# Kernel optimization log

Measured on AMD Instinct MI355X. Metric: run time of the kernel, lower is better.

The kernel has to match this reference:

```python
import math
import jax, jax.numpy as jnp
import numpy as np

B, T, H = 4096, 49, 512

def setup_inputs() -> dict:
    key = jax.random.key(0)
    ks = jax.random.split(key, 13)
    sc = 1.0 / math.sqrt(H)
    return {
        "v": jax.random.normal(ks[0], (B, T, H), dtype=jnp.float32),
        "h": jax.random.normal(ks[1], (B, H), dtype=jnp.float32),
        "s": jax.random.normal(ks[2], (B, H), dtype=jnp.float32),
        "W_h": jax.random.normal(ks[3], (H, H), dtype=jnp.float32) * sc,
        "b_h": jax.random.normal(ks[4], (H,), dtype=jnp.float32) * sc,
        "W_v": jax.random.normal(ks[5], (H, H), dtype=jnp.float32) * sc,
        "b_v": jax.random.normal(ks[6], (H,), dtype=jnp.float32) * sc,
        "w_z": jax.random.normal(ks[7], (H,), dtype=jnp.float32) * sc,
        "b_z": jax.random.normal(ks[8], (), dtype=jnp.float32) * sc,
        "W_s": jax.random.normal(ks[9], (H, H), dtype=jnp.float32) * sc,
        "b_s": jax.random.normal(ks[10], (H,), dtype=jnp.float32) * sc,
        "w_beta": jax.random.normal(ks[11], (H,), dtype=jnp.float32) * sc,
        "b_beta": jax.random.normal(ks[12], (), dtype=jnp.float32) * sc,
    }

def reference(v, h, s, W_h, b_h, W_v, b_v, w_z, b_z, W_s, b_s, w_beta, b_beta):
    # eval mode: dropout is identity
    h_proj = h @ W_h + b_h                                  # [B, H]
    v_proj = jnp.einsum('bth,hk->btk', v, W_v) + b_v        # [B, T, H]
    z = jnp.tanh(h_proj[:, None, :] + v_proj)               # [B, T, H]
    z = jnp.einsum('bth,h->bt', z, w_z) + b_z               # [B, T]
    beta = jnp.tanh((s @ W_s + b_s + h_proj) * math.sqrt(0.5))  # [B, H]
    beta = (beta @ w_beta + b_beta)[:, None]                # [B, 1]
    a = jax.nn.softmax(jnp.concatenate([z, beta], axis=1), axis=1)  # [B, T+1]
    v_ext = jnp.concatenate([v, s[:, None, :]], axis=1)     # [B, T+1, H]
    c = jnp.einsum('bt,bth->bh', a, v_ext)                  # [B, H]
    return c
```

## Files before the change

kernel.cpp:

```cpp
#include <hip/hip_runtime.h>
#include <stdint.h>

#define B_ 4096
#define T_ 49
#define H_ 512
#define BT_ (B_*T_)

typedef __bf16 bf16x8 __attribute__((ext_vector_type(8)));
typedef float  f32x4  __attribute__((ext_vector_type(4)));
typedef unsigned short ushort_;

__device__ __forceinline__ ushort_ f2bf(float f){
  unsigned int u = __float_as_uint(f);
  u += 0x7fffu + ((u >> 16) & 1u);
  return (ushort_)(u >> 16);
}
__device__ __forceinline__ float bf2f(ushort_ u){
  return __uint_as_float(((unsigned int)u) << 16);
}
__device__ __forceinline__ float fast_tanh(float x){
  float e = __expf(2.0f * x);
  return 1.0f - 2.0f * __builtin_amdgcn_rcpf(e + 1.0f);
}

__global__ __launch_bounds__(256) void k_pack3(
    const float* __restrict__ Wv, const float* __restrict__ Wh,
    const float* __restrict__ Ws, ushort_* __restrict__ bpack,
    ushort_* __restrict__ whp, ushort_* __restrict__ wsp){
  const int grp = blockIdx.x >> 7;
  const float* W = (grp==0) ? Wv : (grp==1) ? Wh : Ws;
  ushort_* pack  = (grp==0) ? bpack : (grp==1) ? whp : wsp;
  int idx = (blockIdx.x & 127) * 256 + threadIdx.x;
  int lane = idx & 63;
  int gt   = (idx >> 6) & 31;
  int kk   = idx >> 11;
  int col  = gt*16 + (lane & 15);
  int k0   = kk*32 + (lane >> 4)*8;
  ushort4 lo, hi;
  lo.x = f2bf(W[(k0+0)*H_ + col]);
  lo.y = f2bf(W[(k0+1)*H_ + col]);
  lo.z = f2bf(W[(k0+2)*H_ + col]);
  lo.w = f2bf(W[(k0+3)*H_ + col]);
  hi.x = f2bf(W[(k0+4)*H_ + col]);
  hi.y = f2bf(W[(k0+5)*H_ + col]);
  hi.z = f2bf(W[(k0+6)*H_ + col]);
  hi.w = f2bf(W[(k0+7)*H_ + col]);
  ushort4* dst = (ushort4*)pack;
  dst[idx*2]   = lo;
  dst[idx*2+1] = hi;
}

__global__ __launch_bounds__(256) void k_proj2(
    const float* __restrict__ h, const float* __restrict__ s,
    const ushort_* __restrict__ whp, const ushort_* __restrict__ wsp,
    const float* __restrict__ bh, const float* __restrict__ bs,
    const float* __restrict__ bv, const float* __restrict__ wbeta,
    const float* __restrict__ bbeta_p,
    float* __restrict__ hpb, float* __restrict__ beta)
{
  __shared__ __align__(16) ushort_ hl[16*H_];
  __shared__ __align__(16) ushort_ sl[16*H_];
  __shared__ float zwp[4][16];
  const int tid = threadIdx.x;
  const int w = tid >> 6, lane = tid & 63;
  const int l15 = lane & 15, l4 = lane >> 4;
  const int b0 = blockIdx.x * 16;

  {
    const int r = tid >> 4;
    const float4* hsrc = (const float4*)(h + (size_t)(b0+r)*H_);
    const float4* ssrc = (const float4*)(s + (size_t)(b0+r)*H_);
    #pragma unroll
    for(int p=0;p<8;p++){
      int q  = (tid & 15) + p*16;
      int k0 = q*4;
      float4 fh = hsrc[q];
      float4 fs = ssrc[q];
      int idx = (k0>>5)*512 + ((((k0&31)>>3)<<4) + r)*8 + (k0&7);
      ushort4 uh; uh.x=f2bf(fh.x); uh.y=f2bf(fh.y); uh.z=f2bf(fh.z); uh.w=f2bf(fh.w);
      ushort4 us; us.x=f2bf(fs.x); us.y=f2bf(fs.y); us.z=f2bf(fs.z); us.w=f2bf(fs.w);
      *(ushort4*)&hl[idx] = uh;
      *(ushort4*)&sl[idx] = us;
    }
  }
  __syncthreads();

  const bf16x8* __restrict__ bph = (const bf16x8*)whp;
  const bf16x8* __restrict__ bps = (const bf16x8*)wsp;
  const int bbase = w*512 + lane;

  f32x4 acch[8], accs[8];
  #pragma unroll
  for(int ni=0;ni<8;ni++){ acch[ni]=(f32x4){0,0,0,0}; accs[ni]=(f32x4){0,0,0,0}; }

  #pragma unroll 2
  for(int kk=0;kk<16;kk++){
    bf16x8 ah = *(const bf16x8*)&hl[kk*512 + lane*8];
    bf16x8 as2 = *(const bf16x8*)&sl[kk*512 + lane*8];
    #pragma unroll
    for(int ni=0;ni<8;ni++){
      acch[ni] = __builtin_amdgcn_mfma_f32_16x16x32_bf16(ah,  bph[kk*2048 + bbase + ni*64], acch[ni], 0,0,0);
      accs[ni] = __builtin_amdgcn_mfma_f32_16x16x32_bf16(as2, bps[kk*2048 + bbase + ni*64], accs[ni], 0,0,0);
    }
  }

  float bhv[8], bsv[8], bvv[8], wbv[8];
  #pragma unroll
  for(int ni=0;ni<8;ni++){
    int col = w*128 + ni*16 + l15;
    bhv[ni] = bh[col]; bsv[ni] = bs[col]; bvv[ni] = bv[col]; wbv[ni] = wbeta[col];
  }
  float btsum[4];
  #pragma unroll
  for(int rr=0;rr<4;rr++){
    int row = l4*4 + rr;
    float bsum = 0.f;
    #pragma unroll
    for(int ni=0;ni<8;ni++){
      int col = w*128 + ni*16 + l15;
      float hp = acch[ni][rr] + bhv[ni];
      hpb[(size_t)(b0+row)*H_ + col] = hp + bvv[ni];
      float bt = fast_tanh((accs[ni][rr] + bsv[ni] + hp) * 0.70710678118654752f);
      bsum = fmaf(bt, wbv[ni], bsum);
    }
    btsum[rr] = bsum;
  }
  #pragma unroll
  for(int rr=0;rr<4;rr++){
    btsum[rr] += __shfl_xor(btsum[rr], 1);
    btsum[rr] += __shfl_xor(btsum[rr], 2);
    btsum[rr] += __shfl_xor(btsum[rr], 4);
    btsum[rr] += __shfl_xor(btsum[rr], 8);
    if(l15 == 0) zwp[w][l4*4+rr] = btsum[rr];
  }
  __syncthreads();
  if(tid < 16)
    beta[b0+tid] = zwp[0][tid] + zwp[1][tid] + zwp[2][tid] + zwp[3][tid] + bbeta_p[0];
}

__global__ __launch_bounds__(256, 2) void k_fused(
    const float* __restrict__ v, const ushort_* __restrict__ bpack,
    const float* __restrict__ hpb, const float* __restrict__ wz,
    const float* __restrict__ bz_p, const float* __restrict__ beta,
    const float* __restrict__ s, float* __restrict__ out)
{
  __shared__ __align__(16) ushort_ Av[T_*H_];
  __shared__ float zw[4][64];
  __shared__ float a_s[64];
  const int tid = threadIdx.x;
  const int w = tid >> 6, lane = tid & 63;
  const int l15 = lane & 15, l4 = lane >> 4;
  const int b = blockIdx.x;

  const f32x4* __restrict__ vsrc = (const f32x4*)(v + (size_t)b * T_ * H_);
  const bf16x8* __restrict__ bp = (const bf16x8*)bpack;
  const int bbase = w*256 + lane;

  const int srow = tid >> 4, c4 = tid & 15;
  const int slot = ((c4 >> 1) ^ (srow & 7));
  const int wsub = ((c4 & 1) << 3);
  const bool r48 = (tid < 16);

#define VLOAD(N0,N1,N2,N3, CH) { \
    N0 = __builtin_nontemporal_load(vsrc + (srow     )*128 + (CH)*16 + c4); \
    N1 = __builtin_nontemporal_load(vsrc + (srow + 16)*128 + (CH)*16 + c4); \
    N2 = __builtin_nontemporal_load(vsrc + (srow + 32)*128 + (CH)*16 + c4); \
    if(r48) N3 = __builtin_nontemporal_load(vsrc + 48*128 + (CH)*16 + c4); }

#define SWRITE(N0,N1,N2,N3, CH) { \
    const int cb_ = (CH)*128; ushort4 u_; \
    u_.x=f2bf(N0[0]); u_.y=f2bf(N0[1]); u_.z=f2bf(N0[2]); u_.w=f2bf(N0[3]); \
    *(ushort4*)((char*)Av + (srow   )*1024 + cb_ + (slot<<4) + wsub) = u_; \
    u_.x=f2bf(N1[0]); u_.y=f2bf(N1[1]); u_.z=f2bf(N1[2]); u_.w=f2bf(N1[3]); \
    *(ushort4*)((char*)Av + (srow+16)*1024 + cb_ + (slot<<4) + wsub) = u_; \
    u_.x=f2bf(N2[0]); u_.y=f2bf(N2[1]); u_.z=f2bf(N2[2]); u_.w=f2bf(N2[3]); \
    *(ushort4*)((char*)Av + (srow+32)*1024 + cb_ + (slot<<4) + wsub) = u_; \
    if(r48){ \
      u_.x=f2bf(N3[0]); u_.y=f2bf(N3[1]); u_.z=f2bf(N3[2]); u_.w=f2bf(N3[3]); \
      *(ushort4*)((char*)Av + 48*1024 + cb_ + (slot<<4) + wsub) = u_; } }

#define AFRAG(af, KS) { \
    _Pragma("unroll") \
    for(int mi=0;mi<4;mi++){ \
      int row_ = (mi < 3) ? (mi*16 + l15) : 48; \
      int g_   = ((KS)*4 + l4) ^ (row_ & 7); \
      af[mi] = *(const bf16x8*)((const char*)Av + row_*1024 + (g_<<4)); } }

#define MFMA16(af, bfr) { \
    __builtin_amdgcn_s_setprio(1); \
    _Pragma("unroll") \
    for(int mi=0;mi<4;mi++) \
      _Pragma("unroll") \
      for(int ni=0;ni<4;ni++) \
        acc[mi][ni] = __builtin_amdgcn_mfma_f32_16x16x32_bf16(af[mi], bfr[ni], acc[mi][ni], 0,0,0); \
    __builtin_amdgcn_s_setprio(0); }

  {
    f32x4 A0,A1,A2,A3, B0,B1,B2,B3;
    VLOAD(A0,A1,A2,A3, 0)
    #pragma unroll
    for(int cc=0; cc<4; cc++){
      VLOAD(B0,B1,B2,B3, 2*cc+1)
      SWRITE(A0,A1,A2,A3, 2*cc)
      if(cc < 3) VLOAD(A0,A1,A2,A3, 2*cc+2)
      SWRITE(B0,B1,B2,B3, 2*cc+1)
    }
  }

  f32x4 acc[4][4];
  bf16x8 bq[4][4];
  bf16x8 af2[2][4];

  #pragma unroll
  for(int mi=0;mi<4;mi++)
    #pragma unroll
    for(int ni=0;ni<4;ni++) acc[mi][ni] = (f32x4){0.f,0.f,0.f,0.f};

  #pragma unroll
  for(int p=0;p<4;p++)
    #pragma unroll
    for(int ni=0;ni<4;ni++) bq[p][ni] = bp[p*2048 + bbase + ni*64];

  __syncthreads();

  AFRAG(af2[0], 0)
  #pragma unroll
  for(int kk=0; kk<16; kk++){
    if(kk < 15){ AFRAG(af2[(kk+1)&1], kk+1) }
    MFMA16(af2[kk&1], bq[kk&3])
    if(kk < 12){
      #pragma unroll
      for(int ni=0;ni<4;ni++) bq[kk&3][ni] = bp[(kk+4)*2048 + bbase + ni*64];
    }
  }

  {
    float wzv[4], hp0[4];
    #pragma unroll
    for(int ni=0;ni<4;ni++){
      int col = w*64 + ni*16 + l15;
      wzv[ni] = wz[col];
      hp0[ni] = hpb[(size_t)b*H_ + col];
    }
    float zp[16];
    #pragma unroll
    for(int mi=0;mi<4;mi++)
      #pragma unroll
      for(int r=0;r<4;r++){
        float az = 0.f;
        #pragma unroll
        for(int ni=0;ni<4;ni++)
          az = fmaf(fast_tanh(acc[mi][ni][r] + hp0[ni]), wzv[ni], az);
        zp[mi*4+r] = az;
      }
    #pragma unroll
    for(int i=0;i<16;i++){
      zp[i] += __shfl_xor(zp[i], 1);
      zp[i] += __shfl_xor(zp[i], 2);
      zp[i] += __shfl_xor(zp[i], 4);
      zp[i] += __shfl_xor(zp[i], 8);
    }
    if(l15 == 0){
      #pragma unroll
      for(int mi=0;mi<4;mi++)
        #pragma unroll
        for(int r=0;r<4;r++)
          zw[w][mi*16 + l4*4 + r] = zp[mi*4+r];
    }
  }

  #pragma unroll
  for(int mi=0;mi<4;mi++)
    #pragma unroll
    for(int ni=0;ni<4;ni++) acc[mi][ni] = (f32x4){0.f,0.f,0.f,0.f};

  #pragma unroll
  for(int p=0;p<4;p++)
    #pragma unroll
    for(int ni=0;ni<4;ni++) bq[p][ni] = bp[p*2048 + 1024 + bbase + ni*64];

  AFRAG(af2[0], 0)
  #pragma unroll
  for(int kk=0; kk<16; kk++){
    if(kk < 15){ AFRAG(af2[(kk+1)&1], kk+1) }
    MFMA16(af2[kk&1], bq[kk&3])
    if(kk < 12){
      #pragma unroll
      for(int ni=0;ni<4;ni++) bq[kk&3][ni] = bp[(kk+4)*2048 + 1024 + bbase + ni*64];
    }
  }

  {
    float wzv[4], hp0[4];
    #pragma unroll
    for(int ni=0;ni<4;ni++){
      int col = 256 + w*64 + ni*16 + l15;
      wzv[ni] = wz[col];
      hp0[ni] = hpb[(size_t)b*H_ + col];
    }
    float zp[16];
    #pragma unroll
    for(int mi=0;mi<4;mi++)
      #pragma unroll
      for(int r=0;r<4;r++){
        float az = 0.f;
        #pragma unroll
        for(int ni=0;ni<4;ni++)
          az = fmaf(fast_tanh(acc[mi][ni][r] + hp0[ni]), wzv[ni], az);
        zp[mi*4+r] = az;
      }
    #pragma unroll
    for(int i=0;i<16;i++){
      zp[i] += __shfl_xor(zp[i], 1);
      zp[i] += __shfl_xor(zp[i], 2);
      zp[i] += __shfl_xor(zp[i], 4);
      zp[i] += __shfl_xor(zp[i], 8);
    }
    if(l15 == 0){
      #pragma unroll
      for(int mi=0;mi<4;mi++)
        #pragma unroll
        for(int r=0;r<4;r++)
          zw[w][mi*16 + l4*4 + r] += zp[mi*4+r];
    }
  }
  __syncthreads();

  if(tid < 64){
    float zv;
    if(tid < T_)       zv = zw[0][tid] + zw[1][tid] + zw[2][tid] + zw[3][tid] + bz_p[0];
    else if(tid == T_) zv = beta[b];
    else               zv = -3.0e38f;
    float m = zv;
    #pragma unroll
    for(int off=32;off>=1;off>>=1) m = fmaxf(m, __shfl_xor(m, off));
    float e = (tid <= T_) ? __expf(zv - m) : 0.f;
    float ssum = e;
    #pragma unroll
    for(int off=32;off>=1;off>>=1) ssum += __shfl_xor(ssum, off);
    a_s[tid] = e * __builtin_amdgcn_rcpf(ssum);
  }
  __syncthreads();

  const int n0 = tid * 2;
  float ax = 0.f, ay = 0.f;
  #pragma unroll 7
  for(int t=0;t<T_;t++){
    float at = a_s[t];
    unsigned int u = *(const unsigned int*)((const char*)Av + t*1024
                       + ((((n0>>3) ^ (t&7)))<<4) + ((n0&7)<<1));
    float x = __uint_as_float((u & 0xFFFFu) << 16);
    float y = __uint_as_float(u & 0xFFFF0000u);
    ax = fmaf(at, x, ax);
    ay = fmaf(at, y, ay);
  }
  float a49 = a_s[T_];
  float2 sv = ((const float2*)(s + (size_t)b*H_))[tid];
  ax = fmaf(a49, sv.x, ax);
  ay = fmaf(a49, sv.y, ay);
  float2 res; res.x = ax; res.y = ay;
  ((float2*)(out + (size_t)b*H_))[tid] = res;
}

extern "C" void kernel_launch(void* const* d_in, const int* in_sizes, int n_in,
                              void* d_out, int out_size, void* d_ws, size_t ws_size,
                              hipStream_t stream)
{
  const float* v   = (const float*)d_in[0];
  const float* h   = (const float*)d_in[1];
  const float* s   = (const float*)d_in[2];
  const float* Wh  = (const float*)d_in[3];
  const float* bh  = (const float*)d_in[4];
  const float* Wv  = (const float*)d_in[5];
  const float* bv  = (const float*)d_in[6];
  const float* wz  = (const float*)d_in[7];
  const float* bz  = (const float*)d_in[8];
  const float* Ws  = (const float*)d_in[9];
  const float* bs  = (const float*)d_in[10];
  const float* wb  = (const float*)d_in[11];
  const float* bbet= (const float*)d_in[12];
  float* out = (float*)d_out;

  float* hpb  = (float*)d_ws;
  float* beta = hpb + (size_t)B_*H_;
  ushort_* bpack = (ushort_*)(beta + B_);
  ushort_* whp   = bpack + (size_t)H_*H_;
  ushort_* wsp   = whp   + (size_t)H_*H_;

  k_pack3<<<384, 256, 0, stream>>>(Wv, Wh, Ws, bpack, whp, wsp);
  k_proj2<<<B_/16, 256, 0, stream>>>(h, s, whp, wsp, bh, bs, bv, wb, bbet, hpb, beta);
  k_fused<<<B_, 256, 0, stream>>>(v, bpack, hpb, wz, bz, beta, s, out);
}
```

Measured before the change: 220.3 us.

## Make fused kernel persistent with double-buffered LDS prefetch of next batch's v

Result: slower. 692.5 us (+214.3%).

```diff
diff --git a/kernel.cpp b/kernel.cpp
--- a/kernel.cpp
+++ b/kernel.cpp
@@ -5,6 +5,7 @@
 #define T_ 49
 #define H_ 512
 #define BT_ (B_*T_)
+#define PB_ (T_*H_)
 
 typedef __bf16 bf16x8 __attribute__((ext_vector_type(8)));
 typedef float  f32x4  __attribute__((ext_vector_type(4)));
@@ -138,228 +139,228 @@
     beta[b0+tid] = zwp[0][tid] + zwp[1][tid] + zwp[2][tid] + zwp[3][tid] + bbeta_p[0];
 }
 
-__global__ __launch_bounds__(256, 2) void k_fused(
+__global__ __launch_bounds__(256, 1) void k_fused(
     const float* __restrict__ v, const ushort_* __restrict__ bpack,
     const float* __restrict__ hpb, const float* __restrict__ wz,
     const float* __restrict__ bz_p, const float* __restrict__ beta,
     const float* __restrict__ s, float* __restrict__ out)
 {
-  __shared__ __align__(16) ushort_ Av[T_*H_];
+  __shared__ __align__(16) ushort_ Av[2*PB_];
   __shared__ float zw[4][64];
   __shared__ float a_s[64];
   const int tid = threadIdx.x;
   const int w = tid >> 6, lane = tid & 63;
   const int l15 = lane & 15, l4 = lane >> 4;
-  const int b = blockIdx.x;
-
-  const f32x4* __restrict__ vsrc = (const f32x4*)(v + (size_t)b * T_ * H_);
+  const int blk = blockIdx.x;
+  const bool t128 = (tid < 128);
+
   const bf16x8* __restrict__ bp = (const bf16x8*)bpack;
   const int bbase = w*256 + lane;
 
-  const int srow = tid >> 4, c4 = tid & 15;
-  const int slot = ((c4 >> 1) ^ (srow & 7));
-  const int wsub = ((c4 & 1) << 3);
-  const bool r48 = (tid < 16);
-
-#define VLOAD(N0,N1,N2,N3, CH) { \
-    N0 = __builtin_nontemporal_load(vsrc + (srow     )*128 + (CH)*16 + c4); \
-    N1 = __builtin_nontemporal_load(vsrc + (srow + 16)*128 + (CH)*16 + c4); \
-    N2 = __builtin_nontemporal_load(vsrc + (srow + 32)*128 + (CH)*16 + c4); \
-    if(r48) N3 = __builtin_nontemporal_load(vsrc + 48*128 + (CH)*16 + c4); }
-
-#define SWRITE(N0,N1,N2,N3, CH) { \
-    const int cb_ = (CH)*128; ushort4 u_; \
-    u_.x=f2bf(N0[0]); u_.y=f2bf(N0[1]); u_.z=f2bf(N0[2]); u_.w=f2bf(N0[3]); \
-    *(ushort4*)((char*)Av + (srow   )*1024 + cb_ + (slot<<4) + wsub) = u_; \
-    u_.x=f2bf(N1[0]); u_.y=f2bf(N1[1]); u_.z=f2bf(N1[2]); u_.w=f2bf(N1[3]); \
-    *(ushort4*)((char*)Av + (srow+16)*1024 + cb_ + (slot<<4) + wsub) = u_; \
-    u_.x=f2bf(N2[0]); u_.y=f2bf(N2[1]); u_.z=f2bf(N2[2]); u_.w=f2bf(N2[3]); \
-    *(ushort4*)((char*)Av + (srow+32)*1024 + cb_ + (slot<<4) + wsub) = u_; \
-    if(r48){ \
-      u_.x=f2bf(N3[0]); u_.y=f2bf(N3[1]); u_.z=f2bf(N3[2]); u_.w=f2bf(N3[3]); \
-      *(ushort4*)((char*)Av + 48*1024 + cb_ + (slot<<4) + wsub) = u_; } }
-
-#define AFRAG(af, KS) { \
+  float wzv0[4], wzv1[4];
+  #pragma unroll
+  for(int ni=0;ni<4;ni++){
+    wzv0[ni] = wz[      w*64 + ni*16 + l15];
+    wzv1[ni] = wz[256 + w*64 + ni*16 + l15];
+  }
+  const float bzv = bz_p[0];
+
+#define SIDX(J, VI, WB) { \
+    int flat_ = ((J) < 24) ? (tid + (J)*256) : (6144 + tid); \
+    int row_ = flat_ >> 7, c4_ = flat_ & 127; \
+    VI = row_*128 + c4_; \
+    WB = row_*1024 + ((((c4_>>1) ^ (row_&7)))<<4) + ((c4_&1)<<3); }
+
+#define SISSUE(SR, VS, J0, JN) { \
+    _Pragma("unroll") \
+    for(int j=(J0); j<(JN); j++){ \
+      if(j != 24 || t128){ int vi_, wb_; SIDX(j, vi_, wb_) \
+        SR[j-(J0)] = __builtin_nontemporal_load((VS) + vi_); } } }
+
+#define SWR(SR, DST, J0, A, Bn) { \
+    _Pragma("unroll") \
+    for(int j=(A); j<(Bn); j++){ \
+      if((j+(J0)) != 24 || t128){ int vi_, wb_; SIDX(j+(J0), vi_, wb_) \
+        ushort4 u_; u_.x=f2bf(SR[j][0]); u_.y=f2bf(SR[j][1]); \
+        u_.z=f2bf(SR[j][2]); u_.w=f2bf(SR[j][3]); \
+        *(ushort4*)((DST) + wb_) = u_; } } }
+
+#define AFRAG(af, KS, SRC) { \
     _Pragma("unroll") \
     for(int mi=0;mi<4;mi++){ \
       int row_ = (mi < 3) ? (mi*16 + l15) : 48; \
       int g_   = ((KS)*4 + l4) ^ (row_ & 7); \
-      af[mi] = *(const bf16x8*)((const char*)Av + row_*1024 + (g_<<4)); } }
+      af[mi] = *(const bf16x8*)((SRC) + row_*1024 + (g_<<4)); } }
 
 #define MFMA16(af, bfr) { \
-    __builtin_amdgcn_s_setprio(1); \
     _Pragma("unroll") \
     for(int mi=0;mi<4;mi++) \
       _Pragma("unroll") \
       for(int ni=0;ni<4;ni++) \
-        acc[mi][ni] = __builtin_amdgcn_mfma_f32_16x16x32_bf16(af[mi], bfr[ni], acc[mi][ni], 0,0,0); \
-    __builtin_amdgcn_s_setprio(0); }
+        acc[mi][ni] = __builtin_amdgcn_mfma_f32_16x16x32_bf16(af[mi], bfr[ni], acc[mi][ni], 0,0,0); }
+
+#define BLOADP(DST, KK, P) { \
+    _Pragma("unroll") \
+    for(int ni=0;ni<4;ni++) DST[ni] = bp[(KK)*2048 + (P)*1024 + bbase + ni*64]; }
 
   {
-    f32x4 A0,A1,A2,A3, B0,B1,B2,B3;
-    VLOAD(A0,A1,A2,A3, 0)
-    #pragma unroll
-    for(int cc=0; cc<4; cc++){
-      VLOAD(B0,B1,B2,B3, 2*cc+1)
-      SWRITE(A0,A1,A2,A3, 2*cc)
-      if(cc < 3) VLOAD(A0,A1,A2,A3, 2*cc+2)
-      SWRITE(B0,B1,B2,B3, 2*cc+1)
-    }
-  }
-
-  f32x4 acc[4][4];
-  bf16x8 bq[4][4];
-  bf16x8 af2[2][4];
-
-  #pragma unroll
-  for(int mi=0;mi<4;mi++)
-    #pragma unroll
-    for(int ni=0;ni<4;ni++) acc[mi][ni] = (f32x4){0.f,0.f,0.f,0.f};
-
-  #pragma unroll
-  for(int p=0;p<4;p++)
-    #pragma unroll
-    for(int ni=0;ni<4;ni++) bq[p][ni] = bp[p*2048 + bbase + ni*64];
-
+    const f32x4* vs = (const f32x4*)(v + (size_t)(blk*16)*T_*H_);
+    f32x4 pA[12], pBv[13];
+    SISSUE(pA, vs, 0, 12)
+    SISSUE(pBv, vs, 12, 25)
+    SWR(pA, (char*)Av, 0, 0, 12)
+    SWR(pBv, (char*)Av, 12, 0, 13)
+  }
   __syncthreads();
 
-  AFRAG(af2[0], 0)
-  #pragma unroll
-  for(int kk=0; kk<16; kk++){
-    if(kk < 15){ AFRAG(af2[(kk+1)&1], kk+1) }
-    MFMA16(af2[kk&1], bq[kk&3])
-    if(kk < 12){
-      #pragma unroll
-      for(int ni=0;ni<4;ni++) bq[kk&3][ni] = bp[(kk+4)*2048 + bbase + ni*64];
-    }
-  }
-
-  {
-    float wzv[4], hp0[4];
-    #pragma unroll
-    for(int ni=0;ni<4;ni++){
-      int col = w*64 + ni*16 + l15;
-      wzv[ni] = wz[col];
-      hp0[ni] = hpb[(size_t)b*H_ + col];
-    }
-    float zp[16];
+  #pragma unroll 1
+  for(int bi=0; bi<16; bi++){
+    const int b = blk*16 + bi;
+    const char* curc = (const char*)Av + (bi&1)*(PB_*2);
+    char* nxtc = (char*)Av + ((bi+1)&1)*(PB_*2);
+    const f32x4* vsn = (const f32x4*)(v + (size_t)(b+1)*T_*H_);
+    const bool more = (bi < 15);
+
+    f32x4 srA[12], srB[13];
+    f32x4 acc[4][4];
+    bf16x8 bq[2][4], af2[2][4];
+
     #pragma unroll
     for(int mi=0;mi<4;mi++)
       #pragma unroll
-      for(int r=0;r<4;r++){
-        float az = 0.f;
-        #pragma unroll
-        for(int ni=0;ni<4;ni++)
-          az = fmaf(fast_tanh(acc[mi][ni][r] + hp0[ni]), wzv[ni], az);
-        zp[mi*4+r] = az;
-      }
-    #pragma unroll
-    for(int i=0;i<16;i++){
-      zp[i] += __shfl_xor(zp[i], 1);
-      zp[i] += __shfl_xor(zp[i], 2);
-      zp[i] += __shfl_xor(zp[i], 4);
-      zp[i] += __shfl_xor(zp[i], 8);
-    }
-    if(l15 == 0){
+      for(int ni=0;ni<4;ni++) acc[mi][ni] = (f32x4){0.f,0.f,0.f,0.f};
+    BLOADP(bq[0], 0, 0)
+    BLOADP(bq[1], 1, 0)
+    AFRAG(af2[0], 0, curc)
+
+    #pragma unroll
+    for(int kk=0; kk<16; kk++){
+      if(kk < 15){ AFRAG(af2[(kk+1)&1], kk+1, curc) }
+      if(kk == 2 && more){ SISSUE(srA, vsn, 0, 12) }
+      if(kk == 12 && more){ SISSUE(srB, vsn, 12, 25) }
+      MFMA16(af2[kk&1], bq[kk&1])
+      if(kk < 14){ BLOADP(bq[kk&1], kk+2, 0) }
+      if(kk == 8  && more){ SWR(srA, nxtc, 0, 0, 6) }
+      if(kk == 10 && more){ SWR(srA, nxtc, 0, 6, 12) }
+    }
+
+    {
+      float hpv[4];
+      #pragma unroll
+      for(int ni=0;ni<4;ni++) hpv[ni] = hpb[(size_t)b*H_ + w*64 + ni*16 + l15];
+      float zp[16];
       #pragma unroll
       for(int mi=0;mi<4;mi++)
         #pragma unroll
-        for(int r=0;r<4;r++)
-          zw[w][mi*16 + l4*4 + r] = zp[mi*4+r];
-    }
-  }
-
-  #pragma unroll
-  for(int mi=0;mi<4;mi++)
-    #pragma unroll
-    for(int ni=0;ni<4;ni++) acc[mi][ni] = (f32x4){0.f,0.f,0.f,0.f};
-
-  #pragma unroll
-  for(int p=0;p<4;p++)
-    #pragma unroll
-    for(int ni=0;ni<4;ni++) bq[p][ni] = bp[p*2048 + 1024 + bbase + ni*64];
-
-  AFRAG(af2[0], 0)
-  #pragma unroll
-  for(int kk=0; kk<16; kk++){
-    if(kk < 15){ AFRAG(af2[(kk+1)&1], kk+1) }
-    MFMA16(af2[kk&1], bq[kk&3])
-    if(kk < 12){
-      #pragma unroll
-      for(int ni=0;ni<4;ni++) bq[kk&3][ni] = bp[(kk+4)*2048 + 1024 + bbase + ni*64];
-    }
-  }
-
-  {
-    float wzv[4], hp0[4];
-    #pragma unroll
-    for(int ni=0;ni<4;ni++){
-      int col = 256 + w*64 + ni*16 + l15;
-      wzv[ni] = wz[col];
-      hp0[ni] = hpb[(size_t)b*H_ + col];
-    }
-    float zp[16];
+        for(int r=0;r<4;r++){
+          float az = 0.f;
+          #pragma unroll
+          for(int ni=0;ni<4;ni++)
+            az = fmaf(fast_tanh(acc[mi][ni][r] + hpv[ni]), wzv0[ni], az);
+          zp[mi*4+r] = az;
+        }
+      #pragma unroll
+      for(int i=0;i<16;i++){
+        zp[i] += __shfl_xor(zp[i], 1);
+        zp[i] += __shfl_xor(zp[i], 2);
+        zp[i] += __shfl_xor(zp[i], 4);
+        zp[i] += __shfl_xor(zp[i], 8);
+      }
+      if(l15 == 0){
+        #pragma unroll
+        for(int mi=0;mi<4;mi++)
+          #pragma unroll
+          for(int r=0;r<4;r++)
+            zw[w][mi*16 + l4*4 + r] = zp[mi*4+r];
+      }
+    }
+
     #pragma unroll
     for(int mi=0;mi<4;mi++)
       #pragma unroll
-      for(int r=0;r<4;r++){
-        float az = 0.f;
-        #pragma unroll
-        for(int ni=0;ni<4;ni++)
-          az = fmaf(fast_tanh(acc[mi][ni][r] + hp0[ni]), wzv[ni], az);
-        zp[mi*4+r] = az;
-      }
-    #pragma unroll
-    for(int i=0;i<16;i++){
-      zp[i] += __shfl_xor(zp[i], 1);
-      zp[i] += __shfl_xor(zp[i], 2);
-      zp[i] += __shfl_xor(zp[i], 4);
-      zp[i] += __shfl_xor(zp[i], 8);
-    }
-    if(l15 == 0){
+      for(int ni=0;ni<4;ni++) acc[mi][ni] = (f32x4){0.f,0.f,0.f,0.f};
+    BLOADP(bq[0], 0, 1)
+    BLOADP(bq[1], 1, 1)
+    AFRAG(af2[0], 0, curc)
+
+    #pragma unroll
+    for(int kk=0; kk<16; kk++){
+      if(kk < 15){ AFRAG(af2[(kk+1)&1], kk+1, curc) }
+      MFMA16(af2[kk&1], bq[kk&1])
+      if(kk < 14){ BLOADP(bq[kk&1], kk+2, 1) }
+      if(kk == 2 && more){ SWR(srB, nxtc, 12, 0, 5) }
+      if(kk == 4 && more){ SWR(srB, nxtc, 12, 5, 9) }
+      if(kk == 6 && more){ SWR(srB, nxtc, 12, 9, 13) }
+    }
+
+    {
+      float hpv[4];
+      #pragma unroll
+      for(int ni=0;ni<4;ni++) hpv[ni] = hpb[(size_t)b*H_ + 256 + w*64 + ni*16 + l15];
+      float zp[16];
       #pragma unroll
       for(int mi=0;mi<4;mi++)
         #pragma unroll
-        for(int r=0;r<4;r++)
-          zw[w][mi*16 + l4*4 + r] += zp[mi*4+r];
-    }
-  }
-  __syncthreads();
-
-  if(tid < 64){
-    float zv;
-    if(tid < T_)       zv = zw[0][tid] + zw[1][tid] + zw[2][tid] + zw[3][tid] + bz_p[0];
-    else if(tid == T_) zv = beta[b];
-    else               zv = -3.0e38f;
-    float m = zv;
-    #pragma unroll
-    for(int off=32;off>=1;off>>=1) m = fmaxf(m, __shfl_xor(m, off));
-    float e = (tid <= T_) ? __expf(zv - m) : 0.f;
-    float ssum = e;
-    #pragma unroll
-    for(int off=32;off>=1;off>>=1) ssum += __shfl_xor(ssum, off);
-    a_s[tid] = e * __builtin_amdgcn_rcpf(ssum);
-  }
-  __syncthreads();
-
-  const int n0 = tid * 2;
-  float ax = 0.f, ay = 0.f;
-  #pragma unroll 7
-  for(int t=0;t<T_;t++){
-    float at = a_s[t];
-    unsigned int u = *(const unsigned int*)((const char*)Av + t*1024
-                       + ((((n0>>3) ^ (t&7)))<<4) + ((n0&7)<<1));
-    float x = __uint_as_float((u & 0xFFFFu) << 16);
-    float y = __uint_as_float(u & 0xFFFF0000u);
-    ax = fmaf(at, x, ax);
-    ay = fmaf(at, y, ay);
-  }
-  float a49 = a_s[T_];
-  float2 sv = ((const float2*)(s + (size_t)b*H_))[tid];
-  ax = fmaf(a49, sv.x, ax);
-  ay = fmaf(a49, sv.y, ay);
-  float2 res; res.x = ax; res.y = ay;
-  ((float2*)(out + (size_t)b*H_))[tid] = res;
+        for(int r=0;r<4;r++){
+          float az = 0.f;
+          #pragma unroll
+          for(int ni=0;ni<4;ni++)
+            az = fmaf(fast_tanh(acc[mi][ni][r] + hpv[ni]), wzv1[ni], az);
+          zp[mi*4+r] = az;
+        }
+      #pragma unroll
+      for(int i=0;i<16;i++){
+        zp[i] += __shfl_xor(zp[i], 1);
+        zp[i] += __shfl_xor(zp[i], 2);
+        zp[i] += __shfl_xor(zp[i], 4);
+        zp[i] += __shfl_xor(zp[i], 8);
+      }
+      if(l15 == 0){
+        #pragma unroll
+        for(int mi=0;mi<4;mi++)
+          #pragma unroll
+          for(int r=0;r<4;r++)
+            zw[w][mi*16 + l4*4 + r] += zp[mi*4+r];
+      }
+    }
+    __syncthreads();
+
+    if(tid < 64){
+      float zv;
+      if(tid < T_)       zv = zw[0][tid] + zw[1][tid] + zw[2][tid] + zw[3][tid] + bzv;
+      else if(tid == T_) zv = beta[b];
+      else               zv = -3.0e38f;
+      float m = zv;
+      #pragma unroll
+      for(int off=32;off>=1;off>>=1) m = fmaxf(m, __shfl_xor(m, off));
+      float e = (tid <= T_) ? __expf(zv - m) : 0.f;
+      float ssum = e;
+      #pragma unroll
+      for(int off=32;off>=1;off>>=1) ssum += __shfl_xor(ssum, off);
+      a_s[tid] = e * __builtin_amdgcn_rcpf(ssum);
+    }
+    __syncthreads();
+
+    {
+      const int n0 = tid * 2;
+      float ax = 0.f, ay = 0.f;
+      #pragma unroll 7
+      for(int t=0;t<T_;t++){
+        float at = a_s[t];
+        unsigned int u = *(const unsigned int*)(curc + t*1024
+                           + ((((n0>>3) ^ (t&7)))<<4) + ((n0&7)<<1));
+        ax = fmaf(at, __uint_as_float((u & 0xFFFFu) << 16), ax);
+        ay = fmaf(at, __uint_as_float(u & 0xFFFF0000u), ay);
+      }
+      float a49 = a_s[T_];
+      float2 sv = ((const float2*)(s + (size_t)b*H_))[tid];
+      ax = fmaf(a49, sv.x, ax);
+      ay = fmaf(a49, sv.y, ay);
+      float2 res; res.x = ax; res.y = ay;
+      ((float2*)(out + (size_t)b*H_))[tid] = res;
+    }
+    __syncthreads();
+  }
 }
 
 extern "C" void kernel_launch(void* const* d_in, const int* in_sizes, int n_in,
@@ -389,5 +390,5 @@
 
   k_pack3<<<384, 256, 0, stream>>>(Wv, Wh, Ws, bpack, whp, wsp);
   k_proj2<<<B_/16, 256, 0, stream>>>(h, s, whp, wsp, bh, bs, bv, wb, bbet, hpb, beta);
-  k_fused<<<B_, 256, 0, stream>>>(v, bpack, hpb, wz, bz, beta, s, out);
-}
+  k_fused<<<256, 256, 0, stream>>>(v, bpack, hpb, wz, bz, beta, s, out);
+}
```
